# Kernel optimization log

Hardware: AMD Instinct MI355X
Metric: run time of the kernel (lower is better)

## Reference

```python
import jax, jax.numpy as jnp
import numpy as np
import math

B, S = 2, 2048
D_IN = 512
D_OUT = 512
P = 8
K = 8


def setup_inputs() -> dict:
    key = jax.random.key(0)
    ks = jax.random.split(key, 8)
    mean_phi = math.log(math.sqrt(2.0 / (D_IN * K)))
    mean_w2 = math.log(math.sqrt(2.0 / D_OUT))
    x = jax.random.normal(ks[0], (B, S, D_IN), dtype=jnp.float32)
    phi_raw = mean_phi + 0.2 * jax.random.normal(ks[1], (D_OUT, D_IN * K), dtype=jnp.float32)
    phi_bias = jnp.zeros((D_OUT,), dtype=jnp.float32)
    raw_weight2 = mean_w2 + 0.2 * jax.random.normal(ks[2], (P, D_OUT, D_OUT), dtype=jnp.float32)
    bias2 = jnp.zeros((P, D_OUT), dtype=jnp.float32)
    gate_raw2 = jnp.full((P,), -3.0, dtype=jnp.float32)
    # kaiming_uniform with a=sqrt(5) on shape (P, 2*D_in, D_out): fan_in = 2*D_in
    bound = math.sqrt(6.0 / ((1.0 + 5.0) * (2 * D_IN)))
    z_weight = jax.random.uniform(ks[3], (P, 2 * D_IN, D_OUT), dtype=jnp.float32,
                                  minval=-bound, maxval=bound)
    gate_raw = jnp.full((P,), -3.0, dtype=jnp.float32)
    output_bias = jnp.zeros((P, D_OUT), dtype=jnp.float32)
    return {
        "x": x, "phi_raw": phi_raw, "phi_bias": phi_bias,
        "raw_weight2": raw_weight2, "bias2": bias2, "gate_raw2": gate_raw2,
        "z_weight": z_weight, "gate_raw": gate_raw, "output_bias": output_bias,
    }


def reference(x, phi_raw, phi_bias, raw_weight2, bias2, gate_raw2,
              z_weight, gate_raw, output_bias):
    sp = jax.nn.softplus
    orig = x.shape
    x_flat = x.reshape(-1, D_IN)                              # [N, Din]
    N = x_flat.shape[0]
    shifts = jnp.linspace(-1.0, 1.0, K, dtype=x.dtype)        # [k]
    phi = sp(x_flat[:, :, None] + shifts[None, None, :])      # [N, Din, k]
    phi_flat = phi.reshape(N, D_IN * K)                       # [N, Din*k]
    # PositiveLinearHK: weight = softplus(raw)^2
    w_phi = jnp.square(sp(phi_raw))                           # [Dout, Din*k]
    x_proj = phi_flat @ w_phi.T + phi_bias                    # [N, Dout]
    g1 = jax.nn.sigmoid(gate_raw)[:, None, None]              # [P,1,1]
    z0 = sp(x_proj[None, :, :] * g1)                          # [P, N, Dout]
    w2 = jnp.square(sp(raw_weight2))                          # [P, Dout, Dout]
    # bmm(z0, w2.transpose(1,2)) == einsum over the second Dout axis of w2
    z1 = jnp.einsum('pnd,ped->pne', z0, w2) + bias2[:, None, :]
    g2 = jax.nn.sigmoid(gate_raw2)[:, None, None]
    z1 = sp(z1 * g2)                                          # [P, N, Dout]
    x_res_in = jnp.concatenate([x_flat, x_flat], axis=-1)     # [N, 2*Din]
    x_res = jnp.einsum('nc,pce->pne', x_res_in, z_weight)     # [P, N, Dout]
    z_final = sp(z1 + x_res) + output_bias[:, None, :]        # [P, N, Dout]
    out = jnp.transpose(z_final, (1, 0, 2))                   # [N, P, Dout]
    return out.reshape(tuple(orig[:-1]) + (P, D_OUT))
```

## Files before the change

kernel.cpp:

```cpp
#include <hip/hip_runtime.h>

typedef unsigned short u16;
typedef __attribute__((ext_vector_type(8))) short bf16x8;
typedef __attribute__((ext_vector_type(4))) float floatx4;
typedef __attribute__((ext_vector_type(8))) unsigned short u16x8;
typedef __attribute__((ext_vector_type(4))) unsigned short u16x4;

#define NTOK 4096
#define DDIN 512
#define DDOUT 512
#define NP 8
#define SPLITK 4

__device__ __forceinline__ float b2f(u16 b) {
    union { unsigned int u; float f; } v; v.u = ((unsigned int)b) << 16; return v.f;
}
__device__ __forceinline__ u16 f2b(float f) {
    union { float f; unsigned int u; } v; v.f = f;
    unsigned int r = (v.u + 0x7fffu + ((v.u >> 16) & 1u)) >> 16;
    return (u16)r;
}
__device__ __forceinline__ float sp(float x) {
    return fmaxf(x, 0.f) + __logf(1.f + __expf(-fabsf(x)));
}
__device__ __forceinline__ float sigm(float x) { return 1.f / (1.f + __expf(-x)); }

__device__ __forceinline__ void gld16(const u16* g, u16* l) {
    __builtin_amdgcn_global_load_lds((const __attribute__((address_space(1))) void*)g,
                                     (__attribute__((address_space(3))) void*)l, 16, 0, 0);
}

__global__ void prep_sqsp2(const float* __restrict__ in1, u16* __restrict__ out1, int n1,
                           const float* __restrict__ in2, u16* __restrict__ out2, int n2) {
    int i = blockIdx.x * 256 + threadIdx.x;
    if (i < n1) {
        float s = sp(in1[i]);
        out1[i] = f2b(s * s);
    } else if (i - n1 < n2) {
        int j = i - n1;
        float s = sp(in2[j]);
        out2[j] = f2b(s * s);
    }
}

__global__ void prep_zwT(const float* __restrict__ zw, u16* __restrict__ zwT) {
    int p = blockIdx.z;
    int c0 = blockIdx.x * 32, e0 = blockIdx.y * 32;
    __shared__ float tb[32][33];
    int tx = threadIdx.x, ty = threadIdx.y;
    const float* base = zw + (size_t)p * 1024 * 512;
#pragma unroll
    for (int r = 0; r < 4; ++r) {
        int cl = ty * 4 + r;
        float a = base[(size_t)(c0 + cl) * 512 + e0 + tx];
        float b = base[(size_t)(c0 + cl + 512) * 512 + e0 + tx];
        tb[cl][tx] = a + b;
    }
    __syncthreads();
    u16* outb = zwT + (size_t)p * 512 * 512;
#pragma unroll
    for (int r = 0; r < 4; ++r) {
        int el = ty * 4 + r;
        outb[(size_t)(e0 + el) * 512 + c0 + tx] = f2b(tb[tx][el]);
    }
}

__global__ void phi_kernel(const float* __restrict__ x, u16* __restrict__ phi,
                           u16* __restrict__ xb) {
    int i = blockIdx.x * 256 + threadIdx.x;
    float xv = x[i];
    xb[i] = f2b(xv);
    u16x8 v;
#pragma unroll
    for (int k = 0; k < 8; ++k) {
        float s = -1.f + (2.f / 7.f) * (float)k;
        v[k] = f2b(sp(xv + s));
    }
    *(u16x8*)(phi + (size_t)i * 8) = v;
}


__launch_bounds__(512, 4)
__global__ void gemm1p(const u16* __restrict__ phi, const u16* __restrict__ wphi,
                       u16* __restrict__ xpart) {
    __shared__ __align__(16) u16 lds[2 * 2 * 8192];

    const int id = blockIdx.x;
    const int kc = id & 3;
    const int local = id >> 2;
    const int o0 = (local & 3) * 128;
    const int n0 = (local >> 2) * 128;
    const int kbase = kc * 1024;

    const int t = threadIdx.x;
    const int wave = t >> 6, lane = t & 63;
    const int wm = wave & 1, wn = wave >> 1;
    const int l15 = lane & 15, quad = lane >> 4;
    const int srow = t >> 3;
    const int sgx = ((t & 7) ^ (srow & 7)) * 8;

    const u16* gA = phi  + (size_t)(n0 + srow) * 4096 + kbase + sgx;
    const u16* gB = wphi + (size_t)(o0 + srow) * 4096 + kbase + sgx;

    floatx4 acc[4][2];
#pragma unroll
    for (int i = 0; i < 4; ++i)
#pragma unroll
        for (int j = 0; j < 2; ++j) acc[i][j] = {0.f, 0.f, 0.f, 0.f};

    auto STAGE = [&](int b, int k0) {
        u16* L = lds + b * 16384;
#pragma unroll
        for (int c = 0; c < 2; ++c) {
            gld16(gA + k0 + c * 64 * 4096, L + c * 4096 + t * 8);
            gld16(gB + k0 + c * 64 * 4096, L + 8192 + c * 4096 + t * 8);
        }
    };

    STAGE(0, 0);
    for (int it = 0; it < 16; ++it) {
        const int cur = it & 1;
        __syncthreads();
        if (it < 15) STAGE(cur ^ 1, (it + 1) * 64);
        const u16* As = lds + cur * 16384;
        const u16* Bs = As + 8192;
#pragma unroll
        for (int ks = 0; ks < 2; ++ks) {
            bf16x8 a[4], b[2];
#pragma unroll
            for (int s = 0; s < 4; ++s) {
                int ra = wm * 64 + s * 16 + l15;
                a[s] = *(const bf16x8*)(As + ra * 64 + (((ks * 4 + quad) ^ (ra & 7)) * 8));
            }
#pragma unroll
            for (int s = 0; s < 2; ++s) {
                int rb = wn * 32 + s * 16 + l15;
                b[s] = *(const bf16x8*)(Bs + rb * 64 + (((ks * 4 + quad) ^ (rb & 7)) * 8));
            }
#pragma unroll
            for (int sm = 0; sm < 4; ++sm)
#pragma unroll
                for (int sn = 0; sn < 2; ++sn)
                    acc[sm][sn] = __builtin_amdgcn_mfma_f32_16x16x32_bf16(a[sm], b[sn], acc[sm][sn], 0, 0, 0);
        }
    }

    u16* xp = xpart + (size_t)kc * NTOK * DDOUT;
#pragma unroll
    for (int sm = 0; sm < 4; ++sm)
#pragma unroll
        for (int sn = 0; sn < 2; ++sn) {
            int gcol = o0 + wn * 32 + sn * 16 + l15;
#pragma unroll
            for (int r = 0; r < 4; ++r) {
                int grow = n0 + wm * 64 + sm * 16 + quad * 4 + r;
                xp[(size_t)grow * DDOUT + gcol] = f2b(acc[sm][sn][r]);
            }
        }
}

__global__ void reduce_ep(const u16* __restrict__ xpart, const float* __restrict__ phi_bias,
                          const float* __restrict__ gate_raw, u16* __restrict__ z0) {
    int idx = blockIdx.x * 256 + threadIdx.x;
    int n = idx >> 7;
    int o4 = (idx & 127) * 4;
    size_t base = (size_t)n * DDOUT + o4;
    float s0 = 0.f, s1 = 0.f, s2 = 0.f, s3 = 0.f;
#pragma unroll
    for (int kc = 0; kc < SPLITK; ++kc) {
        u16x4 v = *(const u16x4*)(xpart + (size_t)kc * NTOK * DDOUT + base);
        s0 += b2f(v[0]); s1 += b2f(v[1]); s2 += b2f(v[2]); s3 += b2f(v[3]);
    }
    floatx4 pb = *(const floatx4*)(phi_bias + o4);
    s0 += pb[0]; s1 += pb[1]; s2 += pb[2]; s3 += pb[3];
#pragma unroll
    for (int p = 0; p < NP; ++p) {
        float g = sigm(gate_raw[p]);
        u16x4 v;
        v[0] = f2b(sp(s0 * g)); v[1] = f2b(sp(s1 * g));
        v[2] = f2b(sp(s2 * g)); v[3] = f2b(sp(s3 * g));
        *(u16x4*)(z0 + (size_t)p * NTOK * DDOUT + base) = v;
    }
}

__launch_bounds__(512, 2)
__global__ void gemm23(const u16* __restrict__ z0, const u16* __restrict__ w2b,
                       const u16* __restrict__ xb, const u16* __restrict__ zwT,
                       const float* __restrict__ bias2, const float* __restrict__ gate_raw2,
                       const float* __restrict__ output_bias, float* __restrict__ out) {
    __shared__ __align__(16) u16 lds[2 * 4 * 8192];

    const int id = blockIdx.x;
    const int p = id & 7;
    const int local = id >> 3;
    const int e0 = (local & 3) * 128;
    const int n0 = (local >> 2) * 128;

    const int t = threadIdx.x;
    const int wave = t >> 6, lane = t & 63;
    const int wm = wave & 1, wn = wave >> 1;
    const int l15 = lane & 15, quad = lane >> 4;
    const int srow = t >> 3;
    const int sgx = ((t & 7) ^ (srow & 7)) * 8;

    const u16* gA1 = z0  + (size_t)p * NTOK * DDOUT + (size_t)(n0 + srow) * 512 + sgx;
    const u16* gB1 = w2b + (size_t)p * DDOUT * DDOUT + (size_t)(e0 + srow) * 512 + sgx;
    const u16* gA2 = xb  + (size_t)(n0 + srow) * 512 + sgx;
    const u16* gB2 = zwT + (size_t)p * DDOUT * DDIN + (size_t)(e0 + srow) * 512 + sgx;

    floatx4 acc1[4][2], acc2[4][2];
#pragma unroll
    for (int i = 0; i < 4; ++i)
#pragma unroll
        for (int j = 0; j < 2; ++j) {
            acc1[i][j] = {0.f, 0.f, 0.f, 0.f};
            acc2[i][j] = {0.f, 0.f, 0.f, 0.f};
        }

    auto STAGE = [&](int b, int k0) {
        u16* L = lds + b * 32768;
#pragma unroll
        for (int c = 0; c < 2; ++c) {
            gld16(gA1 + k0 + c * 64 * 512, L + c * 4096 + t * 8);
            gld16(gB1 + k0 + c * 64 * 512, L + 8192 + c * 4096 + t * 8);
            gld16(gA2 + k0 + c * 64 * 512, L + 16384 + c * 4096 + t * 8);
            gld16(gB2 + k0 + c * 64 * 512, L + 24576 + c * 4096 + t * 8);
        }
    };

    STAGE(0, 0);
    for (int it = 0; it < 8; ++it) {
        const int cur = it & 1;
        __syncthreads();
        if (it < 7) STAGE(cur ^ 1, (it + 1) * 64);
        const u16* A1 = lds + cur * 32768;
        const u16* B1 = A1 + 8192;
        const u16* A2 = A1 + 16384;
        const u16* B2 = A1 + 24576;
#pragma unroll
        for (int ks = 0; ks < 2; ++ks) {
            bf16x8 a1[4], b1[2], a2[4], b2[2];
#pragma unroll
            for (int s = 0; s < 4; ++s) {
                int ra = wm * 64 + s * 16 + l15;
                int ko = ((ks * 4 + quad) ^ (ra & 7)) * 8;
                a1[s] = *(const bf16x8*)(A1 + ra * 64 + ko);
                a2[s] = *(const bf16x8*)(A2 + ra * 64 + ko);
            }
#pragma unroll
            for (int s = 0; s < 2; ++s) {
                int rb = wn * 32 + s * 16 + l15;
                int ko = ((ks * 4 + quad) ^ (rb & 7)) * 8;
                b1[s] = *(const bf16x8*)(B1 + rb * 64 + ko);
                b2[s] = *(const bf16x8*)(B2 + rb * 64 + ko);
            }
#pragma unroll
            for (int sm = 0; sm < 4; ++sm)
#pragma unroll
                for (int sn = 0; sn < 2; ++sn) {
                    acc1[sm][sn] = __builtin_amdgcn_mfma_f32_16x16x32_bf16(a1[sm], b1[sn], acc1[sm][sn], 0, 0, 0);
                    acc2[sm][sn] = __builtin_amdgcn_mfma_f32_16x16x32_bf16(a2[sm], b2[sn], acc2[sm][sn], 0, 0, 0);
                }
        }
    }

    const float g2p = sigm(gate_raw2[p]);
#pragma unroll
    for (int sm = 0; sm < 4; ++sm)
#pragma unroll
        for (int sn = 0; sn < 2; ++sn) {
            int gcol = e0 + wn * 32 + sn * 16 + l15;
            float bb = bias2[p * DDOUT + gcol];
            float ob = output_bias[p * DDOUT + gcol];
#pragma unroll
            for (int r = 0; r < 4; ++r) {
                int grow = n0 + wm * 64 + sm * 16 + quad * 4 + r;
                float v1 = acc1[sm][sn][r] + bb;
                float o = sp(sp(v1 * g2p) + acc2[sm][sn][r]) + ob;
                out[(size_t)grow * (NP * DDOUT) + p * DDOUT + gcol] = o;
            }
        }
}

extern "C" void kernel_launch(void* const* d_in, const int* in_sizes, int n_in,
                              void* d_out, int out_size, void* d_ws, size_t ws_size,
                              hipStream_t stream) {
    const float* x           = (const float*)d_in[0];
    const float* phi_raw     = (const float*)d_in[1];
    const float* phi_bias    = (const float*)d_in[2];
    const float* raw_weight2 = (const float*)d_in[3];
    const float* bias2       = (const float*)d_in[4];
    const float* gate_raw2   = (const float*)d_in[5];
    const float* z_weight    = (const float*)d_in[6];
    const float* gate_raw    = (const float*)d_in[7];
    const float* output_bias = (const float*)d_in[8];
    float* out = (float*)d_out;

    u16* ws   = (u16*)d_ws;
    u16* phi  = ws;
    u16* wphi = phi + (size_t)4096 * 4096;
    u16* w2b  = wphi + (size_t)512 * 4096;
    u16* zwT  = w2b + (size_t)8 * 512 * 512;
    u16* z0   = zwT + (size_t)8 * 512 * 512;
    u16* xb   = z0 + (size_t)8 * 4096 * 512;
    u16* xpart = (u16*)d_out;

    const int n1 = 512 * 4096, n2 = 8 * 512 * 512;
    hipLaunchKernelGGL(prep_sqsp2, dim3((n1 + n2) / 256), dim3(256), 0, stream,
                       phi_raw, wphi, n1, raw_weight2, w2b, n2);
    hipLaunchKernelGGL(prep_zwT, dim3(16, 16, 8), dim3(32, 8), 0, stream, z_weight, zwT);
    hipLaunchKernelGGL(phi_kernel, dim3(8192), dim3(256), 0, stream, x, phi, xb);
    hipLaunchKernelGGL(gemm1p, dim3(512), dim3(512), 0, stream, phi, wphi, xpart);
    hipLaunchKernelGGL(reduce_ep, dim3(2048), dim3(256), 0, stream, xpart, phi_bias, gate_raw, z0);
    hipLaunchKernelGGL(gemm23, dim3(1024), dim3(512), 0, stream,
                       z0, w2b, xb, zwT, bias2, gate_raw2, output_bias, out);
}
```

Before: 210.7 us.

## Widen gemm1 tile to full output width with 8-way split-K and triple buffering

The first GEMM now has each block compute a 128x512 output tile, covering the full output width, instead of 128x128. The phi activation tile is therefore loaded once per block rather than by four column blocks, which cuts the dominant global read of the 32MB phi matrix. Split-K goes from 4 to 8 and the grid shrinks to 256 blocks, and the K loop uses a three-stage LDS ring driven by explicit vmcnt waits and barriers in place of __syncthreads double buffering. The costs are 128 accumulator floats per thread with lower occupancy, and twice as many bf16 partial sums written and then read by the reduction kernel.

After: 216.8 us. 1.03x slower.

```diff
diff --git a/kernel.cpp b/kernel.cpp
--- a/kernel.cpp
+++ b/kernel.cpp
@@ -10,7 +10,7 @@
 #define DDIN 512
 #define DDOUT 512
 #define NP 8
-#define SPLITK 4
+#define SPLITK 8
 
 __device__ __forceinline__ float b2f(u16 b) {
     union { unsigned int u; float f; } v; v.u = ((unsigned int)b) << 16; return v.f;
@@ -29,6 +29,11 @@
     __builtin_amdgcn_global_load_lds((const __attribute__((address_space(1))) void*)g,
                                      (__attribute__((address_space(3))) void*)l, 16, 0, 0);
 }
+
+#define WAITBAR(N) do { \
+    asm volatile("s_waitcnt vmcnt(" N ")\n\ts_barrier" ::: "memory"); \
+    __builtin_amdgcn_sched_barrier(0); \
+} while (0)
 
 __global__ void prep_sqsp2(const float* __restrict__ in1, u16* __restrict__ out1, int n1,
                            const float* __restrict__ in2, u16* __restrict__ out2, int n2) {
@@ -79,78 +84,85 @@
     *(u16x8*)(phi + (size_t)i * 8) = v;
 }
 
-
-__launch_bounds__(512, 4)
+__launch_bounds__(512, 2)
 __global__ void gemm1p(const u16* __restrict__ phi, const u16* __restrict__ wphi,
                        u16* __restrict__ xpart) {
-    __shared__ __align__(16) u16 lds[2 * 2 * 8192];
+    __shared__ __align__(16) u16 lds[3 * 20480];
 
     const int id = blockIdx.x;
-    const int kc = id & 3;
-    const int local = id >> 2;
-    const int o0 = (local & 3) * 128;
-    const int n0 = (local >> 2) * 128;
-    const int kbase = kc * 1024;
+    const int kc = id & 7;
+    const int n0 = (id >> 3) * 128;
+    const int kbase = kc * 512;
 
     const int t = threadIdx.x;
     const int wave = t >> 6, lane = t & 63;
     const int wm = wave & 1, wn = wave >> 1;
     const int l15 = lane & 15, quad = lane >> 4;
-    const int srow = t >> 3;
-    const int sgx = ((t & 7) ^ (srow & 7)) * 8;
-
-    const u16* gA = phi  + (size_t)(n0 + srow) * 4096 + kbase + sgx;
-    const u16* gB = wphi + (size_t)(o0 + srow) * 4096 + kbase + sgx;
-
-    floatx4 acc[4][2];
+    const int sgx = ((t & 3) ^ ((t >> 3) & 3)) * 8;
+
+    const u16* gA = phi  + (size_t)(n0 + (t >> 2)) * 4096 + kbase + sgx;
+    const u16* gB = wphi + (size_t)(t >> 2) * 4096 + kbase + sgx;
+
+    floatx4 acc[4][8];
 #pragma unroll
     for (int i = 0; i < 4; ++i)
 #pragma unroll
-        for (int j = 0; j < 2; ++j) acc[i][j] = {0.f, 0.f, 0.f, 0.f};
+        for (int j = 0; j < 8; ++j) acc[i][j] = {0.f, 0.f, 0.f, 0.f};
 
     auto STAGE = [&](int b, int k0) {
-        u16* L = lds + b * 16384;
-#pragma unroll
-        for (int c = 0; c < 2; ++c) {
-            gld16(gA + k0 + c * 64 * 4096, L + c * 4096 + t * 8);
-            gld16(gB + k0 + c * 64 * 4096, L + 8192 + c * 4096 + t * 8);
-        }
+        u16* L = lds + b * 20480;
+        gld16(gA + k0, L + t * 8);
+#pragma unroll
+        for (int c = 0; c < 4; ++c)
+            gld16(gB + k0 + (size_t)c * 128 * 4096, L + 4096 + c * 4096 + t * 8);
     };
 
+    const int ko = (quad ^ ((l15 >> 1) & 3)) * 8;
+
+    auto COMPUTE = [&](int b) {
+        const u16* A = lds + b * 20480;
+        const u16* B = A + 4096;
+        bf16x8 a[4];
+#pragma unroll
+        for (int s = 0; s < 4; ++s)
+            a[s] = *(const bf16x8*)(A + (wm * 64 + s * 16 + l15) * 32 + ko);
+#pragma unroll
+        for (int h = 0; h < 2; ++h) {
+            bf16x8 bb[4];
+#pragma unroll
+            for (int s = 0; s < 4; ++s)
+                bb[s] = *(const bf16x8*)(B + (wn * 128 + (h * 4 + s) * 16 + l15) * 32 + ko);
+#pragma unroll
+            for (int sm = 0; sm < 4; ++sm)
+#pragma unroll
+                for (int sn = 0; sn < 4; ++sn)
+                    acc[sm][h * 4 + sn] = __builtin_amdgcn_mfma_f32_16x16x32_bf16(
+                        a[sm], bb[sn], acc[sm][h * 4 + sn], 0, 0, 0);
+        }
+    };
+
     STAGE(0, 0);
-    for (int it = 0; it < 16; ++it) {
-        const int cur = it & 1;
-        __syncthreads();
-        if (it < 15) STAGE(cur ^ 1, (it + 1) * 64);
-        const u16* As = lds + cur * 16384;
-        const u16* Bs = As + 8192;
-#pragma unroll
-        for (int ks = 0; ks < 2; ++ks) {
-            bf16x8 a[4], b[2];
-#pragma unroll
-            for (int s = 0; s < 4; ++s) {
-                int ra = wm * 64 + s * 16 + l15;
-                a[s] = *(const bf16x8*)(As + ra * 64 + (((ks * 4 + quad) ^ (ra & 7)) * 8));
-            }
-#pragma unroll
-            for (int s = 0; s < 2; ++s) {
-                int rb = wn * 32 + s * 16 + l15;
-                b[s] = *(const bf16x8*)(Bs + rb * 64 + (((ks * 4 + quad) ^ (rb & 7)) * 8));
-            }
-#pragma unroll
-            for (int sm = 0; sm < 4; ++sm)
-#pragma unroll
-                for (int sn = 0; sn < 2; ++sn)
-                    acc[sm][sn] = __builtin_amdgcn_mfma_f32_16x16x32_bf16(a[sm], b[sn], acc[sm][sn], 0, 0, 0);
-        }
-    }
+    STAGE(1, 32);
+    int bs = 2, bc = 0, k0 = 64;
+    for (int it = 0; it < 15; ++it) {
+        WAITBAR("5");
+        if (it < 14) {
+            STAGE(bs, k0);
+            k0 += 32;
+            if (++bs == 3) bs = 0;
+        }
+        COMPUTE(bc);
+        if (++bc == 3) bc = 0;
+    }
+    WAITBAR("0");
+    COMPUTE(bc);
 
     u16* xp = xpart + (size_t)kc * NTOK * DDOUT;
 #pragma unroll
     for (int sm = 0; sm < 4; ++sm)
 #pragma unroll
-        for (int sn = 0; sn < 2; ++sn) {
-            int gcol = o0 + wn * 32 + sn * 16 + l15;
+        for (int sn = 0; sn < 8; ++sn) {
+            int gcol = wn * 128 + sn * 16 + l15;
 #pragma unroll
             for (int r = 0; r < 4; ++r) {
                 int grow = n0 + wm * 64 + sm * 16 + quad * 4 + r;
@@ -310,7 +322,7 @@
                        phi_raw, wphi, n1, raw_weight2, w2b, n2);
     hipLaunchKernelGGL(prep_zwT, dim3(16, 16, 8), dim3(32, 8), 0, stream, z_weight, zwT);
     hipLaunchKernelGGL(phi_kernel, dim3(8192), dim3(256), 0, stream, x, phi, xb);
-    hipLaunchKernelGGL(gemm1p, dim3(512), dim3(512), 0, stream, phi, wphi, xpart);
+    hipLaunchKernelGGL(gemm1p, dim3(256), dim3(512), 0, stream, phi, wphi, xpart);
     hipLaunchKernelGGL(reduce_ep, dim3(2048), dim3(256), 0, stream, xpart, phi_bias, gate_raw, z0);
     hipLaunchKernelGGL(gemm23, dim3(1024), dim3(512), 0, stream,
                        z0, w2b, xb, zwT, bias2, gate_raw2, output_bias, out);
```

## Remove split-K in first GEMM and fuse bias/gate/softplus epilogue

Applied to the files above, without the earlier changes.

Replaces the split-K first GEMM plus separate reduction kernel with a single full-K GEMM that applies bias, per-path sigmoid gates and softplus directly, writing z0. This removes the partial-sum buffer round trip and one kernel launch. It reduces the grid from 512 to 128 blocks, leaving many CUs idle and lengthening each block's K loop, and moves the eight-way epilogue into fewer threads.

Result: slower. 233.5 us (+10.8%).

```diff
diff --git a/kernel.cpp b/kernel.cpp
--- a/kernel.cpp
+++ b/kernel.cpp
@@ -10,7 +10,6 @@
 #define DDIN 512
 #define DDOUT 512
 #define NP 8
-#define SPLITK 4
 
 __device__ __forceinline__ float b2f(u16 b) {
     union { unsigned int u; float f; } v; v.u = ((unsigned int)b) << 16; return v.f;
@@ -79,18 +78,15 @@
     *(u16x8*)(phi + (size_t)i * 8) = v;
 }
 
-
-__launch_bounds__(512, 4)
-__global__ void gemm1p(const u16* __restrict__ phi, const u16* __restrict__ wphi,
-                       u16* __restrict__ xpart) {
+__launch_bounds__(512, 2)
+__global__ void gemm1z(const u16* __restrict__ phi, const u16* __restrict__ wphi,
+                       const float* __restrict__ phi_bias, const float* __restrict__ gate_raw,
+                       u16* __restrict__ z0) {
     __shared__ __align__(16) u16 lds[2 * 2 * 8192];
 
     const int id = blockIdx.x;
-    const int kc = id & 3;
-    const int local = id >> 2;
-    const int o0 = (local & 3) * 128;
-    const int n0 = (local >> 2) * 128;
-    const int kbase = kc * 1024;
+    const int n0 = (id & 31) * 128;
+    const int o0 = (id >> 5) * 128;
 
     const int t = threadIdx.x;
     const int wave = t >> 6, lane = t & 63;
@@ -99,8 +95,8 @@
     const int srow = t >> 3;
     const int sgx = ((t & 7) ^ (srow & 7)) * 8;
 
-    const u16* gA = phi  + (size_t)(n0 + srow) * 4096 + kbase + sgx;
-    const u16* gB = wphi + (size_t)(o0 + srow) * 4096 + kbase + sgx;
+    const u16* gA = phi  + (size_t)(n0 + srow) * 4096 + sgx;
+    const u16* gB = wphi + (size_t)(o0 + srow) * 4096 + sgx;
 
     floatx4 acc[4][2];
 #pragma unroll
@@ -112,16 +108,16 @@
         u16* L = lds + b * 16384;
 #pragma unroll
         for (int c = 0; c < 2; ++c) {
-            gld16(gA + k0 + c * 64 * 4096, L + c * 4096 + t * 8);
-            gld16(gB + k0 + c * 64 * 4096, L + 8192 + c * 4096 + t * 8);
+            gld16(gA + k0 + (size_t)c * 64 * 4096, L + c * 4096 + t * 8);
+            gld16(gB + k0 + (size_t)c * 64 * 4096, L + 8192 + c * 4096 + t * 8);
         }
     };
 
     STAGE(0, 0);
-    for (int it = 0; it < 16; ++it) {
+    for (int it = 0; it < 64; ++it) {
         const int cur = it & 1;
         __syncthreads();
-        if (it < 15) STAGE(cur ^ 1, (it + 1) * 64);
+        if (it < 63) STAGE(cur ^ 1, (it + 1) * 64);
         const u16* As = lds + cur * 16384;
         const u16* Bs = As + 8192;
 #pragma unroll
@@ -145,42 +141,26 @@
         }
     }
 
-    u16* xp = xpart + (size_t)kc * NTOK * DDOUT;
+    float g[NP];
+#pragma unroll
+    for (int p = 0; p < NP; ++p) g[p] = sigm(gate_raw[p]);
+
 #pragma unroll
     for (int sm = 0; sm < 4; ++sm)
 #pragma unroll
         for (int sn = 0; sn < 2; ++sn) {
             int gcol = o0 + wn * 32 + sn * 16 + l15;
+            float pb = phi_bias[gcol];
 #pragma unroll
             for (int r = 0; r < 4; ++r) {
                 int grow = n0 + wm * 64 + sm * 16 + quad * 4 + r;
-                xp[(size_t)grow * DDOUT + gcol] = f2b(acc[sm][sn][r]);
-            }
-        }
-}
-
-__global__ void reduce_ep(const u16* __restrict__ xpart, const float* __restrict__ phi_bias,
-                          const float* __restrict__ gate_raw, u16* __restrict__ z0) {
-    int idx = blockIdx.x * 256 + threadIdx.x;
-    int n = idx >> 7;
-    int o4 = (idx & 127) * 4;
-    size_t base = (size_t)n * DDOUT + o4;
-    float s0 = 0.f, s1 = 0.f, s2 = 0.f, s3 = 0.f;
-#pragma unroll
-    for (int kc = 0; kc < SPLITK; ++kc) {
-        u16x4 v = *(const u16x4*)(xpart + (size_t)kc * NTOK * DDOUT + base);
-        s0 += b2f(v[0]); s1 += b2f(v[1]); s2 += b2f(v[2]); s3 += b2f(v[3]);
-    }
-    floatx4 pb = *(const floatx4*)(phi_bias + o4);
-    s0 += pb[0]; s1 += pb[1]; s2 += pb[2]; s3 += pb[3];
-#pragma unroll
-    for (int p = 0; p < NP; ++p) {
-        float g = sigm(gate_raw[p]);
-        u16x4 v;
-        v[0] = f2b(sp(s0 * g)); v[1] = f2b(sp(s1 * g));
-        v[2] = f2b(sp(s2 * g)); v[3] = f2b(sp(s3 * g));
-        *(u16x4*)(z0 + (size_t)p * NTOK * DDOUT + base) = v;
-    }
+                float v = acc[sm][sn][r] + pb;
+                size_t base = (size_t)grow * DDOUT + gcol;
+#pragma unroll
+                for (int p = 0; p < NP; ++p)
+                    z0[(size_t)p * NTOK * DDOUT + base] = f2b(sp(v * g[p]));
+            }
+        }
 }
 
 __launch_bounds__(512, 2)
@@ -303,15 +283,14 @@
     u16* zwT  = w2b + (size_t)8 * 512 * 512;
     u16* z0   = zwT + (size_t)8 * 512 * 512;
     u16* xb   = z0 + (size_t)8 * 4096 * 512;
-    u16* xpart = (u16*)d_out;
 
     const int n1 = 512 * 4096, n2 = 8 * 512 * 512;
     hipLaunchKernelGGL(prep_sqsp2, dim3((n1 + n2) / 256), dim3(256), 0, stream,
                        phi_raw, wphi, n1, raw_weight2, w2b, n2);
     hipLaunchKernelGGL(prep_zwT, dim3(16, 16, 8), dim3(32, 8), 0, stream, z_weight, zwT);
     hipLaunchKernelGGL(phi_kernel, dim3(8192), dim3(256), 0, stream, x, phi, xb);
-    hipLaunchKernelGGL(gemm1p, dim3(512), dim3(512), 0, stream, phi, wphi, xpart);
-    hipLaunchKernelGGL(reduce_ep, dim3(2048), dim3(256), 0, stream, xpart, phi_bias, gate_raw, z0);
+    hipLaunchKernelGGL(gemm1z, dim3(128), dim3(512), 0, stream,
+                       phi, wphi, phi_bias, gate_raw, z0);
     hipLaunchKernelGGL(gemm23, dim3(1024), dim3(512), 0, stream,
                        z0, w2b, xb, zwT, bias2, gate_raw2, output_bias, out);
 }
```

## Fuse prep kernels and retile gemm1 with split-K of eight

Applied to the files above, without the earlier changes.

Merges the three preprocessing kernels into one launch that dispatches on block index. Gemm1 moves to split-K 8 with 256-thread blocks, 4x4 MFMA tiles per wave and single-buffered LDS staging with two barriers per step. This cuts launch count and raises gemm1 occupancy and per-wave reuse. In exchange it drops the double-buffer overlap and doubles the partial-sum traffic reduce_ep has to read back. The xpart buffer in d_out must now hold 8 partial slices.

Result: slower. 216.6 us (+2.8%).

```diff
diff --git a/kernel.cpp b/kernel.cpp
--- a/kernel.cpp
+++ b/kernel.cpp
@@ -10,7 +10,7 @@
 #define DDIN 512
 #define DDOUT 512
 #define NP 8
-#define SPLITK 4
+#define SPLITK 8
 
 __device__ __forceinline__ float b2f(u16 b) {
     union { unsigned int u; float f; } v; v.u = ((unsigned int)b) << 16; return v.f;
@@ -30,117 +30,107 @@
                                      (__attribute__((address_space(3))) void*)l, 16, 0, 0);
 }
 
-__global__ void prep_sqsp2(const float* __restrict__ in1, u16* __restrict__ out1, int n1,
-                           const float* __restrict__ in2, u16* __restrict__ out2, int n2) {
-    int i = blockIdx.x * 256 + threadIdx.x;
-    if (i < n1) {
-        float s = sp(in1[i]);
-        out1[i] = f2b(s * s);
-    } else if (i - n1 < n2) {
-        int j = i - n1;
-        float s = sp(in2[j]);
-        out2[j] = f2b(s * s);
-    }
-}
-
-__global__ void prep_zwT(const float* __restrict__ zw, u16* __restrict__ zwT) {
-    int p = blockIdx.z;
-    int c0 = blockIdx.x * 32, e0 = blockIdx.y * 32;
-    __shared__ float tb[32][33];
-    int tx = threadIdx.x, ty = threadIdx.y;
-    const float* base = zw + (size_t)p * 1024 * 512;
-#pragma unroll
-    for (int r = 0; r < 4; ++r) {
-        int cl = ty * 4 + r;
-        float a = base[(size_t)(c0 + cl) * 512 + e0 + tx];
-        float b = base[(size_t)(c0 + cl + 512) * 512 + e0 + tx];
-        tb[cl][tx] = a + b;
-    }
-    __syncthreads();
-    u16* outb = zwT + (size_t)p * 512 * 512;
-#pragma unroll
-    for (int r = 0; r < 4; ++r) {
-        int el = ty * 4 + r;
-        outb[(size_t)(e0 + el) * 512 + c0 + tx] = f2b(tb[tx][el]);
-    }
-}
-
-__global__ void phi_kernel(const float* __restrict__ x, u16* __restrict__ phi,
-                           u16* __restrict__ xb) {
-    int i = blockIdx.x * 256 + threadIdx.x;
-    float xv = x[i];
-    xb[i] = f2b(xv);
-    u16x8 v;
-#pragma unroll
-    for (int k = 0; k < 8; ++k) {
-        float s = -1.f + (2.f / 7.f) * (float)k;
-        v[k] = f2b(sp(xv + s));
-    }
-    *(u16x8*)(phi + (size_t)i * 8) = v;
-}
-
-
-__launch_bounds__(512, 4)
+__global__ void prep_fused(const float* __restrict__ phi_raw, u16* __restrict__ wphi,
+                           const float* __restrict__ raw_weight2, u16* __restrict__ w2b,
+                           const float* __restrict__ x, u16* __restrict__ phi,
+                           u16* __restrict__ xb,
+                           const float* __restrict__ zw, u16* __restrict__ zwT) {
+    const int b = blockIdx.x;
+    const int t = threadIdx.x;
+    if (b < 8192) {
+        int i = b * 256 + t;
+        float s = sp(phi_raw[i]);
+        wphi[i] = f2b(s * s);
+    } else if (b < 16384) {
+        int i = (b - 8192) * 256 + t;
+        float s = sp(raw_weight2[i]);
+        w2b[i] = f2b(s * s);
+    } else if (b < 24576) {
+        int i = (b - 16384) * 256 + t;
+        float xv = x[i];
+        xb[i] = f2b(xv);
+        u16x8 v;
+#pragma unroll
+        for (int k = 0; k < 8; ++k) {
+            float s = -1.f + (2.f / 7.f) * (float)k;
+            v[k] = f2b(sp(xv + s));
+        }
+        *(u16x8*)(phi + (size_t)i * 8) = v;
+    } else {
+        __shared__ float tb[32][33];
+        int i = b - 24576;
+        int p = i >> 8;
+        int c0 = (i & 15) * 32, e0 = ((i >> 4) & 15) * 32;
+        int tx = t & 31, ty = t >> 5;
+        const float* base = zw + (size_t)p * 1024 * 512;
+#pragma unroll
+        for (int r = 0; r < 4; ++r) {
+            int cl = ty * 4 + r;
+            float a = base[(size_t)(c0 + cl) * 512 + e0 + tx];
+            float bb = base[(size_t)(c0 + cl + 512) * 512 + e0 + tx];
+            tb[cl][tx] = a + bb;
+        }
+        __syncthreads();
+        u16* outb = zwT + (size_t)p * 512 * 512;
+#pragma unroll
+        for (int r = 0; r < 4; ++r) {
+            int el = ty * 4 + r;
+            outb[(size_t)(e0 + el) * 512 + c0 + tx] = f2b(tb[tx][el]);
+        }
+    }
+}
+
+__launch_bounds__(256, 3)
 __global__ void gemm1p(const u16* __restrict__ phi, const u16* __restrict__ wphi,
                        u16* __restrict__ xpart) {
-    __shared__ __align__(16) u16 lds[2 * 2 * 8192];
+    __shared__ __align__(16) u16 lds[2 * 8192];
+    u16* As = lds;
+    u16* Bs = lds + 8192;
 
     const int id = blockIdx.x;
-    const int kc = id & 3;
-    const int local = id >> 2;
+    const int kc = id & 7;
+    const int local = id >> 3;
     const int o0 = (local & 3) * 128;
     const int n0 = (local >> 2) * 128;
-    const int kbase = kc * 1024;
+    const int kbase = kc * 512;
 
     const int t = threadIdx.x;
     const int wave = t >> 6, lane = t & 63;
-    const int wm = wave & 1, wn = wave >> 1;
+    const int wm = wave >> 1, wn = wave & 1;
     const int l15 = lane & 15, quad = lane >> 4;
     const int srow = t >> 3;
-    const int sgx = ((t & 7) ^ (srow & 7)) * 8;
-
-    const u16* gA = phi  + (size_t)(n0 + srow) * 4096 + kbase + sgx;
-    const u16* gB = wphi + (size_t)(o0 + srow) * 4096 + kbase + sgx;
-
-    floatx4 acc[4][2];
+    const int sgx = (((t & 7) ^ (srow & 7))) * 8;
+
+    floatx4 acc[4][4];
 #pragma unroll
     for (int i = 0; i < 4; ++i)
 #pragma unroll
-        for (int j = 0; j < 2; ++j) acc[i][j] = {0.f, 0.f, 0.f, 0.f};
-
-    auto STAGE = [&](int b, int k0) {
-        u16* L = lds + b * 16384;
-#pragma unroll
-        for (int c = 0; c < 2; ++c) {
-            gld16(gA + k0 + c * 64 * 4096, L + c * 4096 + t * 8);
-            gld16(gB + k0 + c * 64 * 4096, L + 8192 + c * 4096 + t * 8);
-        }
-    };
-
-    STAGE(0, 0);
-    for (int it = 0; it < 16; ++it) {
-        const int cur = it & 1;
+        for (int j = 0; j < 4; ++j) acc[i][j] = {0.f, 0.f, 0.f, 0.f};
+
+    for (int k0 = 0; k0 < 512; k0 += 64) {
+        const u16* ga = phi + (size_t)(n0 + srow) * 4096 + kbase + k0 + sgx;
+        const u16* gb = wphi + (size_t)(o0 + srow) * 4096 + kbase + k0 + sgx;
         __syncthreads();
-        if (it < 15) STAGE(cur ^ 1, (it + 1) * 64);
-        const u16* As = lds + cur * 16384;
-        const u16* Bs = As + 8192;
+#pragma unroll
+        for (int c = 0; c < 4; ++c) {
+            gld16(ga + (size_t)c * 32 * 4096, As + c * 2048 + t * 8);
+            gld16(gb + (size_t)c * 32 * 4096, Bs + c * 2048 + t * 8);
+        }
+        __syncthreads();
 #pragma unroll
         for (int ks = 0; ks < 2; ++ks) {
-            bf16x8 a[4], b[2];
+            bf16x8 a[4], b[4];
 #pragma unroll
             for (int s = 0; s < 4; ++s) {
                 int ra = wm * 64 + s * 16 + l15;
+                int rb = wn * 64 + s * 16 + l15;
                 a[s] = *(const bf16x8*)(As + ra * 64 + (((ks * 4 + quad) ^ (ra & 7)) * 8));
-            }
-#pragma unroll
-            for (int s = 0; s < 2; ++s) {
-                int rb = wn * 32 + s * 16 + l15;
                 b[s] = *(const bf16x8*)(Bs + rb * 64 + (((ks * 4 + quad) ^ (rb & 7)) * 8));
             }
 #pragma unroll
             for (int sm = 0; sm < 4; ++sm)
 #pragma unroll
-                for (int sn = 0; sn < 2; ++sn)
+                for (int sn = 0; sn < 4; ++sn)
                     acc[sm][sn] = __builtin_amdgcn_mfma_f32_16x16x32_bf16(a[sm], b[sn], acc[sm][sn], 0, 0, 0);
         }
     }
@@ -149,8 +139,8 @@
 #pragma unroll
     for (int sm = 0; sm < 4; ++sm)
 #pragma unroll
-        for (int sn = 0; sn < 2; ++sn) {
-            int gcol = o0 + wn * 32 + sn * 16 + l15;
+        for (int sn = 0; sn < 4; ++sn) {
+            int gcol = o0 + wn * 64 + sn * 16 + l15;
 #pragma unroll
             for (int r = 0; r < 4; ++r) {
                 int grow = n0 + wm * 64 + sm * 16 + quad * 4 + r;
@@ -305,12 +295,9 @@
     u16* xb   = z0 + (size_t)8 * 4096 * 512;
     u16* xpart = (u16*)d_out;
 
-    const int n1 = 512 * 4096, n2 = 8 * 512 * 512;
-    hipLaunchKernelGGL(prep_sqsp2, dim3((n1 + n2) / 256), dim3(256), 0, stream,
-                       phi_raw, wphi, n1, raw_weight2, w2b, n2);
-    hipLaunchKernelGGL(prep_zwT, dim3(16, 16, 8), dim3(32, 8), 0, stream, z_weight, zwT);
-    hipLaunchKernelGGL(phi_kernel, dim3(8192), dim3(256), 0, stream, x, phi, xb);
-    hipLaunchKernelGGL(gemm1p, dim3(512), dim3(512), 0, stream, phi, wphi, xpart);
+    hipLaunchKernelGGL(prep_fused, dim3(26624), dim3(256), 0, stream,
+                       phi_raw, wphi, raw_weight2, w2b, x, phi, xb, z_weight, zwT);
+    hipLaunchKernelGGL(gemm1p, dim3(1024), dim3(256), 0, stream, phi, wphi, xpart);
     hipLaunchKernelGGL(reduce_ep, dim3(2048), dim3(256), 0, stream, xpart, phi_bias, gate_raw, z0);
     hipLaunchKernelGGL(gemm23, dim3(1024), dim3(512), 0, stream,
                        z0, w2b, xb, zwT, bias2, gate_raw2, output_bias, out);
```
